# Optimization experiments

Measured on AMD Instinct MI355X. Metric: run time of the kernel, lower is better.

Reference implementation:

```python
import jax, jax.numpy as jnp
import numpy as np

N, E, C_IN, W = 7936, 63488, 5, 64
K, H1, H2 = 8, 64, 16  # kernel size, tgc hidden, gcn out

def _conv1d(x, w, b):
    # x: [N, Cin, L], w: [Cout, Cin, K] -> [N, Cout, L-K+1]
    y = jax.lax.conv_general_dilated(x, w, (1,), 'VALID',
                                     dimension_numbers=('NCH', 'OIH', 'NCH'))
    return y + b[None, :, None]

def _gated_conv(x, w, b, out_ch):
    # Conv1d to 2*out_ch channels, then GLU: P * sigmoid(Q)
    y = _conv1d(x, w, b)
    return y[:, :out_ch] * jax.nn.sigmoid(y[:, out_ch:])

def _gcn(x, edge_index, edge_weight, Wg, bg, num_nodes):
    # x: [T, N, F] (node_dim=-2), GCNConv with self-loops and symmetric norm
    row, col = edge_index[0], edge_index[1]
    loop = jnp.arange(num_nodes, dtype=edge_index.dtype)
    row = jnp.concatenate([row, loop])
    col = jnp.concatenate([col, loop])
    ew = jnp.concatenate([edge_weight, jnp.ones((num_nodes,), x.dtype)])
    deg = jax.ops.segment_sum(ew, col, num_segments=num_nodes)
    dinv = jnp.where(deg > 0, jax.lax.rsqrt(deg), 0.0)
    norm = dinv[row] * ew * dinv[col]              # [E+N]
    xt = jnp.einsum('tnf,fo->tno', x, Wg)          # transform first (F->O)
    msgs = jnp.take(xt, row, axis=1) * norm[None, :, None]  # [T, E+N, O]
    T = x.shape[0]
    out = jnp.zeros((T, num_nodes, Wg.shape[1]), x.dtype).at[:, col, :].add(msgs)
    return out + bg

def setup_inputs() -> dict:
    key = jax.random.key(0)
    ks = jax.random.split(key, 10)
    x = jax.random.normal(ks[0], (N, C_IN, W), jnp.float32)
    edge_index = jax.random.randint(ks[1], (2, E), 0, N, jnp.int64)
    edge_attr = jax.random.uniform(ks[2], (E,), jnp.float32)
    batch = jax.random.randint(ks[3], (N,), 0, 128, jnp.int64)
    s1 = 1.0 / np.sqrt(C_IN * K)
    Wc1 = jax.random.uniform(ks[4], (2 * H1, C_IN, K), jnp.float32, -s1, s1)
    b1 = jax.random.uniform(ks[5], (2 * H1,), jnp.float32, -s1, s1)
    sg = 1.0 / np.sqrt(H1)
    Wg = jax.random.uniform(ks[6], (H1, H2), jnp.float32, -sg, sg)
    bg = jnp.zeros((H2,), jnp.float32)
    s2 = 1.0 / np.sqrt(H2 * K)
    Wc2 = jax.random.uniform(ks[7], (2 * H1, H2, K), jnp.float32, -s2, s2)
    b2 = jax.random.uniform(ks[8], (2 * H1,), jnp.float32, -s2, s2)
    return {'x': x, 'edge_index': edge_index, 'edge_attr': edge_attr,
            'batch': batch, 'Wc1': Wc1, 'b1': b1, 'Wg': Wg, 'bg': bg,
            'Wc2': Wc2, 'b2': b2}

def reference(x, edge_index, edge_attr, batch, Wc1, b1, Wg, bg, Wc2, b2):
    h = _gated_conv(x, Wc1, b1, H1)                # [N, 64, T1]
    h = jnp.transpose(h, (2, 0, 1))                # 'ec cs wc -> wc ec cs'
    h = jax.nn.relu(_gcn(h, edge_index, edge_attr, Wg, bg, x.shape[0]))
    h = jnp.transpose(h, (1, 2, 0))                # 'wc ec cs -> ec cs wc'
    return _gated_conv(h, Wc2, b2, H1)             # [N, 64, T2]
```

## Files before the change

### kernel.cpp

```cpp
#include <hip/hip_runtime.h>
#include <hip/hip_bf16.h>

#define NN 7936
#define EE 63488
#define CIN 5
#define WW 64
#define KK 8
#define H1C 64
#define H2C 16
#define T1 57
#define T2 50
#define FT (T1*H2C)
#define CAP 64
#define GSTR 24

typedef _Float16 half8 __attribute__((ext_vector_type(8)));
typedef _Float16 half4v __attribute__((ext_vector_type(4)));
typedef float f32x4 __attribute__((ext_vector_type(4)));

__device__ __forceinline__ int block_flag(const int* __restrict__ ei,
                                          int* sflag) {
    if (threadIdx.x < 64) {
        int bad = (threadIdx.x < 32) ? (ei[2 * threadIdx.x + 1] != 0) : 0;
        unsigned long long b = __ballot(bad);
        if (threadIdx.x == 0) *sflag = (b == 0ULL) ? 1 : 0;
    }
    __syncthreads();
    return *sflag;
}

__device__ __forceinline__ int load_row(const int* ei, int f, int e) {
    return f ? ei[2 * e] : ei[e];
}
__device__ __forceinline__ int load_col(const int* ei, int f, int e) {
    return f ? ei[2 * (EE + e)] : ei[EE + e];
}

__global__ void k_init(float* __restrict__ deg,
                       const float* __restrict__ Wc2, _Float16* __restrict__ w2p,
                       const float* __restrict__ Wc1, _Float16* __restrict__ w1p,
                       const float* __restrict__ Wg, _Float16* __restrict__ wgp) {
    int b = blockIdx.x;
    if (b < 62) {
        ((int*)deg)[b * 256 + threadIdx.x] = 0;
        return;
    }
    int i = (b - 62) * 256 + threadIdx.x;
    if (i < 16384) {
        int e = i & 7;
        int slot = i >> 3;
        int c  = slot & 15;
        int nt = (slot >> 4) & 7;
        int g  = (slot >> 7) & 3;
        int s  = (slot >> 9) & 3;
        int ci = g * 4 + (e & 3);
        w2p[i] = (_Float16)Wc2[(nt * 16 + c) * 128 + ci * 8 + 2 * s + (e >> 2)];
    } else if (i < 16384 + 8192) {
        int j = i - 16384;
        int e = j & 7;
        int m = (j >> 3) & 127;
        int slg = j >> 10;
        int ci = (slg >> 2) * 4 + (slg & 3);
        int hi = m >> 6;
        int mb = m & 63;
        int mt = mb >> 4, r = mb & 15;
        int sig = hi * 64 + 32 * (mt >> 1) + 8 * (r >> 2) + 4 * (mt & 1) + (r & 3);
        w1p[j] = (ci < CIN) ? (_Float16)Wc1[sig * (CIN * KK) + ci * KK + e]
                            : (_Float16)0.0f;
    } else if (i < 16384 + 8192 + 1024) {
        int j = i - 16384 - 8192;
        int e = j & 7;
        int f = (j >> 3) & 15;
        int slg = j >> 7;
        int c = (slg >> 2) * 32 + (slg & 3) * 8 + e;
        wgp[j] = (_Float16)Wg[c * H2C + f];
    }
}

__global__ __launch_bounds__(256, 3) void k_conv1_fill(
        const float* __restrict__ x, const _Float16* __restrict__ w1p,
        const float* __restrict__ b1, const _Float16* __restrict__ wgp,
        _Float16* __restrict__ xt,
        const int* __restrict__ ei,
        const float* __restrict__ ew, float* __restrict__ deg,
        int* __restrict__ cnt, int2* __restrict__ em) {
    if (blockIdx.x >= NN / 4) {
        __shared__ int sflag;
        int f = block_flag(ei, &sflag);
        int e = (blockIdx.x - NN / 4) * 256 + threadIdx.x;
        if (e < EE) {
            int c = load_col(ei, f, e);
            int r = load_row(ei, f, e);
            float wv = ew[e];
            int pos = atomicAdd(&cnt[c], 1);
            atomicAdd(&deg[c], wv);
            if (pos < CAP)
                em[(c << 6) + pos] = make_int2(r, __float_as_int(wv));
        }
        return;
    }
    int tid = threadIdx.x;
    int w = tid >> 6, lane = tid & 63;
    int lc = lane & 15, lg = lane >> 4;
    int n = blockIdx.x * 4 + w;
    const float* xg = x + (size_t)n * (CIN * WW);

    const half8* w1v = (const half8*)w1p;
    const half8* wgv = (const half8*)wgp;

    half8 av[2][8];
#pragma unroll
    for (int s = 0; s < 2; ++s)
#pragma unroll
        for (int mt = 0; mt < 8; ++mt)
            av[s][mt] = w1v[(s * 4 + lg) * 128 + mt * 16 + lc];
    half8 bw[2];
#pragma unroll
    for (int s2 = 0; s2 < 2; ++s2) bw[s2] = wgv[(s2 * 4 + lg) * 16 + lc];

    const float* xr0 = xg + (size_t)lg * WW;
    const float* xr1 = xg + (size_t)(4 + lg) * WW;
    bool cok1 = (4 + lg) < CIN;

    f32x4 acc2[4];
#pragma unroll
    for (int mt2 = 0; mt2 < 4; ++mt2) acc2[mt2] = (f32x4)0.0f;

#pragma unroll
    for (int nt = 0; nt < 4; ++nt) {
        int t = nt * 16 + lc;
        half8 bf0, bf1;
#pragma unroll
        for (int e = 0; e < 8; ++e) {
            int tp = t + e;
            bf0[e] = (_Float16)((tp < WW) ? xr0[tp] : 0.0f);
            bf1[e] = (_Float16)((cok1 && tp < WW) ? xr1[tp] : 0.0f);
        }
        f32x4 acc[8];
#pragma unroll
        for (int mt = 0; mt < 8; ++mt) acc[mt] = (f32x4)0.0f;
#pragma unroll
        for (int mt = 0; mt < 8; ++mt)
            acc[mt] = __builtin_amdgcn_mfma_f32_16x16x32_f16(av[0][mt], bf0,
                                                             acc[mt], 0, 0, 0);
#pragma unroll
        for (int mt = 0; mt < 8; ++mt)
            acc[mt] = __builtin_amdgcn_mfma_f32_16x16x32_f16(av[1][mt], bf1,
                                                             acc[mt], 0, 0, 0);
        half4v h4[4];
#pragma unroll
        for (int mtp = 0; mtp < 4; ++mtp) {
            int cb = 32 * (mtp >> 1) + 8 * lg + 4 * (mtp & 1);
            float4 bP = *(const float4*)(b1 + cb);
            float4 bQ = *(const float4*)(b1 + 64 + cb);
            f32x4 P = acc[mtp];
            f32x4 Q = acc[mtp + 4];
            half4v hh;
            hh[0] = (_Float16)((P[0] + bP.x) * (1.0f / (1.0f + __expf(-(Q[0] + bQ.x)))));
            hh[1] = (_Float16)((P[1] + bP.y) * (1.0f / (1.0f + __expf(-(Q[1] + bQ.y)))));
            hh[2] = (_Float16)((P[2] + bP.z) * (1.0f / (1.0f + __expf(-(Q[2] + bQ.z)))));
            hh[3] = (_Float16)((P[3] + bP.w) * (1.0f / (1.0f + __expf(-(Q[3] + bQ.w)))));
            h4[mtp] = hh;
        }
#pragma unroll
        for (int s2 = 0; s2 < 2; ++s2) {
            half8 af = __builtin_shufflevector(h4[2 * s2], h4[2 * s2 + 1],
                                               0, 1, 2, 3, 4, 5, 6, 7);
            acc2[nt] = __builtin_amdgcn_mfma_f32_16x16x32_f16(af, bw[s2],
                                                              acc2[nt], 0, 0, 0);
        }
    }

    _Float16* xtn = xt + (size_t)n * FT;
#pragma unroll
    for (int mt2 = 0; mt2 < 4; ++mt2) {
#pragma unroll
        for (int j = 0; j < 4; ++j) {
            int t = mt2 * 16 + 4 * lg + j;
            if (t < T1) xtn[t * 16 + lc] = (_Float16)acc2[mt2][j];
        }
    }
}

__global__ __launch_bounds__(256, 4) void k_gc2(
        const _Float16* __restrict__ xt, const float* __restrict__ deg,
        const int* __restrict__ cnt, const int2* __restrict__ em,
        const float* __restrict__ bg, const _Float16* __restrict__ w2p,
        const float* __restrict__ b2, float* __restrict__ out) {
    __shared__ __align__(16) _Float16 gs2[2][58 * GSTR];
    __shared__ __align__(16) float gout[4][16 * T2];
    int tid = threadIdx.x;
    int w = tid >> 6, lane = tid & 63;
    int lc = lane & 15, lg = lane >> 4;
    int nb = w >> 1, h = w & 1;
    int n = blockIdx.x * 2 + nb;
    bool act = (h == 0) || (lane < 50);
    int idx = (h << 6) + lane;

    float dc = rsqrtf(deg[n] + 1.0f);
    float a[8];
    {
        const half8* xs = (const half8*)(xt + (size_t)n * FT);
        half8 u = (half8)(_Float16)0.0f;
        if (act) u = xs[idx];
#pragma unroll
        for (int j = 0; j < 8; ++j) a[j] = (float)u[j] * dc;
    }
    int beg = n << 6;
    int m = min(cnt[n], CAP);
    int2 rw0 = make_int2(0, 0), rw1 = make_int2(0, 0);
    float dg0 = 0.0f, dg1 = 0.0f;
    half8 c0 = (half8)(_Float16)0.0f;
    if (m > 0) {
        rw0 = em[beg];
        dg0 = deg[rw0.x];
        const half8* xr = (const half8*)(xt + (size_t)rw0.x * FT);
        if (act) c0 = xr[idx];
    }
    if (m > 1) { rw1 = em[beg + 1]; dg1 = deg[rw1.x]; }
    for (int i = 0; i < m; ++i) {
        float wv = __int_as_float(rw0.y) * rsqrtf(dg0 + 1.0f);
        half8 d0 = c0;
        int2 rwn = rw1;
        float dgn = dg1;
        if (i + 2 < m) { rwn = em[beg + i + 2]; dgn = deg[rwn.x]; }
        if (i + 1 < m) {
            const half8* xr = (const half8*)(xt + (size_t)rw1.x * FT);
            c0 = (half8)(_Float16)0.0f;
            if (act) c0 = xr[idx];
        }
        rw0 = rw1; dg0 = dg1; rw1 = rwn; dg1 = dgn;
#pragma unroll
        for (int j = 0; j < 8; ++j) a[j] += (float)d0[j] * wv;
    }

    {
        _Float16* g = gs2[nb];
        int f0 = (lane & 1) * 8;
        int t0 = idx >> 1;
        float4 bgA = *(const float4*)(bg + f0);
        float4 bgB = *(const float4*)(bg + f0 + 4);
        float bv[8] = {bgA.x, bgA.y, bgA.z, bgA.w, bgB.x, bgB.y, bgB.z, bgB.w};
        half8 h0;
#pragma unroll
        for (int j = 0; j < 8; ++j)
            h0[j] = (_Float16)fmaxf(a[j] * dc + bv[j], 0.0f);
        if (act) *(half8*)(g + t0 * GSTR + f0) = h0;
    }
    __syncthreads();

    const _Float16* g = gs2[nb];
    half8 af[4][4];
#pragma unroll
    for (int s = 0; s < 4; ++s)
#pragma unroll
        for (int mt = 0; mt < 4; ++mt) {
            int tb = mt * 16 + lc + 2 * s;
            half4v lo = *(const half4v*)(g + tb * GSTR + lg * 4);
            half4v hh = *(const half4v*)(g + (tb + 1) * GSTR + lg * 4);
            af[s][mt] = __builtin_shufflevector(lo, hh, 0, 1, 2, 3, 4, 5, 6, 7);
        }

    const half8* wsv = (const half8*)w2p;
    float* outn = out + (size_t)n * (H1C * T2);
    float* go = gout[w];
#pragma unroll
    for (int np2 = 0; np2 < 2; ++np2) {
        int ntp = (h << 1) + np2;
        f32x4 aP[4], aQ[4];
#pragma unroll
        for (int mt = 0; mt < 4; ++mt) { aP[mt] = (f32x4)0.0f; aQ[mt] = (f32x4)0.0f; }
#pragma unroll
        for (int s = 0; s < 4; ++s) {
            half8 bP = wsv[(s * 4 + lg) * 128 + ntp * 16 + lc];
            half8 bQ = wsv[(s * 4 + lg) * 128 + (ntp + 4) * 16 + lc];
#pragma unroll
            for (int mt = 0; mt < 4; ++mt) {
                aP[mt] = __builtin_amdgcn_mfma_f32_16x16x32_f16(af[s][mt], bP,
                                                                aP[mt], 0, 0, 0);
                aQ[mt] = __builtin_amdgcn_mfma_f32_16x16x32_f16(af[s][mt], bQ,
                                                                aQ[mt], 0, 0, 0);
            }
        }
        int c = ntp * 16 + lc;
        float bp = b2[c], bq = b2[64 + c];
#pragma unroll
        for (int mt = 0; mt < 4; ++mt) {
#pragma unroll
            for (int e2 = 0; e2 < 4; ++e2) {
                int t = mt * 16 + lg * 4 + e2;
                if (t < T2) {
                    float vv = (aP[mt][e2] + bp) *
                               (1.0f / (1.0f + __expf(-(aQ[mt][e2] + bq))));
                    go[lc * T2 + t] = vv;
                }
            }
        }
        float* dst = outn + ntp * (16 * T2);
#pragma unroll
        for (int i = 0; i < 3; ++i) {
            f32x4 v = *(const f32x4*)(go + i * 256 + lane * 4);
            __builtin_nontemporal_store(v, (f32x4*)(dst + i * 256 + lane * 4));
        }
        if (lane < 8) {
            f32x4 v = *(const f32x4*)(go + 768 + lane * 4);
            __builtin_nontemporal_store(v, (f32x4*)(dst + 768 + lane * 4));
        }
    }
}

extern "C" void kernel_launch(void* const* d_in, const int* in_sizes, int n_in,
                              void* d_out, int out_size, void* d_ws, size_t ws_size,
                              hipStream_t stream) {
    const float* x   = (const float*)d_in[0];
    const int*   ei  = (const int*)d_in[1];
    const float* ea  = (const float*)d_in[2];
    const float* Wc1 = (const float*)d_in[4];
    const float* b1  = (const float*)d_in[5];
    const float* Wg  = (const float*)d_in[6];
    const float* bg  = (const float*)d_in[7];
    const float* Wc2 = (const float*)d_in[8];
    const float* b2  = (const float*)d_in[9];
    float* out = (float*)d_out;

    char* ws = (char*)d_ws;
    size_t off = 0;
    auto alloc = [&](size_t bytes) -> void* {
        void* p = ws + off;
        off += (bytes + 255) & ~(size_t)255;
        return p;
    };
    float*    deg = (float*)alloc((size_t)NN * 4);
    int*      cnt = (int*)alloc((size_t)NN * 4);
    int2*     em  = (int2*)alloc((size_t)NN * CAP * 8);
    _Float16* xt  = (_Float16*)alloc((size_t)NN * FT * 2);
    _Float16* w2p = (_Float16*)alloc((size_t)16384 * 2);
    _Float16* w1p = (_Float16*)alloc((size_t)8192 * 2);
    _Float16* wgp = (_Float16*)alloc((size_t)1024 * 2);
    (void)ws_size; (void)in_sizes; (void)n_in; (void)out_size;

    k_init<<<162, 256, 0, stream>>>(deg, Wc2, w2p, Wc1, w1p, Wg, wgp);
    k_conv1_fill<<<NN / 4 + EE / 256, 256, 0, stream>>>(x, w1p, b1, wgp, xt,
                                                        ei, ea, deg, cnt, em);
    k_gc2<<<NN / 2, 256, 0, stream>>>(xt, deg, cnt, em, bg, w2p, b2, out);
}
```

Before: 104.1 us.

## Read conv1/GCN weights directly in fill kernel, shrink gc2 blocks to one node

The fp16 repacking of Wc1 and Wg moves out of the init kernel. The conv1 kernel now loads and converts those weights straight from the fp32 inputs, which makes the init kernel smaller and drops two workspace buffers. The gather/conv2 kernel now runs one node per 128-thread block instead of two nodes per 256-thread block, with fewer LDS bytes per block and a higher occupancy hint. It also raises wave priority around the MFMA loop. The trade-off is redundant per-wave weight conversion in conv1 and twice as many small blocks for gc2.

```diff
diff --git a/kernel.cpp b/kernel.cpp
--- a/kernel.cpp
+++ b/kernel.cpp
@@ -37,49 +37,26 @@
 }
 
 __global__ void k_init(float* __restrict__ deg,
-                       const float* __restrict__ Wc2, _Float16* __restrict__ w2p,
-                       const float* __restrict__ Wc1, _Float16* __restrict__ w1p,
-                       const float* __restrict__ Wg, _Float16* __restrict__ wgp) {
+                       const float* __restrict__ Wc2, _Float16* __restrict__ w2p) {
     int b = blockIdx.x;
     if (b < 62) {
         ((int*)deg)[b * 256 + threadIdx.x] = 0;
         return;
     }
     int i = (b - 62) * 256 + threadIdx.x;
-    if (i < 16384) {
-        int e = i & 7;
-        int slot = i >> 3;
-        int c  = slot & 15;
-        int nt = (slot >> 4) & 7;
-        int g  = (slot >> 7) & 3;
-        int s  = (slot >> 9) & 3;
-        int ci = g * 4 + (e & 3);
-        w2p[i] = (_Float16)Wc2[(nt * 16 + c) * 128 + ci * 8 + 2 * s + (e >> 2)];
-    } else if (i < 16384 + 8192) {
-        int j = i - 16384;
-        int e = j & 7;
-        int m = (j >> 3) & 127;
-        int slg = j >> 10;
-        int ci = (slg >> 2) * 4 + (slg & 3);
-        int hi = m >> 6;
-        int mb = m & 63;
-        int mt = mb >> 4, r = mb & 15;
-        int sig = hi * 64 + 32 * (mt >> 1) + 8 * (r >> 2) + 4 * (mt & 1) + (r & 3);
-        w1p[j] = (ci < CIN) ? (_Float16)Wc1[sig * (CIN * KK) + ci * KK + e]
-                            : (_Float16)0.0f;
-    } else if (i < 16384 + 8192 + 1024) {
-        int j = i - 16384 - 8192;
-        int e = j & 7;
-        int f = (j >> 3) & 15;
-        int slg = j >> 7;
-        int c = (slg >> 2) * 32 + (slg & 3) * 8 + e;
-        wgp[j] = (_Float16)Wg[c * H2C + f];
-    }
+    int e = i & 7;
+    int slot = i >> 3;
+    int c  = slot & 15;
+    int nt = (slot >> 4) & 7;
+    int g  = (slot >> 7) & 3;
+    int s  = (slot >> 9) & 3;
+    int ci = g * 4 + (e & 3);
+    w2p[i] = (_Float16)Wc2[(nt * 16 + c) * 128 + ci * 8 + 2 * s + (e >> 2)];
 }
 
 __global__ __launch_bounds__(256, 3) void k_conv1_fill(
-        const float* __restrict__ x, const _Float16* __restrict__ w1p,
-        const float* __restrict__ b1, const _Float16* __restrict__ wgp,
+        const float* __restrict__ x, const float* __restrict__ Wc1,
+        const float* __restrict__ b1, const float* __restrict__ Wg,
         _Float16* __restrict__ xt,
         const int* __restrict__ ei,
         const float* __restrict__ ew, float* __restrict__ deg,
@@ -105,18 +82,37 @@
     int n = blockIdx.x * 4 + w;
     const float* xg = x + (size_t)n * (CIN * WW);
 
-    const half8* w1v = (const half8*)w1p;
-    const half8* wgv = (const half8*)wgp;
-
     half8 av[2][8];
 #pragma unroll
-    for (int s = 0; s < 2; ++s)
-#pragma unroll
-        for (int mt = 0; mt < 8; ++mt)
-            av[s][mt] = w1v[(s * 4 + lg) * 128 + mt * 16 + lc];
+    for (int s = 0; s < 2; ++s) {
+        int ci = s * 4 + lg;
+#pragma unroll
+        for (int mt = 0; mt < 8; ++mt) {
+            half8 v = (half8)(_Float16)0.0f;
+            if (ci < CIN) {
+                int mb = mt & 3;
+                int sig = (mt >> 2) * 64 + 32 * (mb >> 1) + 8 * (lc >> 2) +
+                          4 * (mb & 1) + (lc & 3);
+                const float* wr = Wc1 + sig * (CIN * KK) + ci * KK;
+                float4 fA = *(const float4*)(wr);
+                float4 fB = *(const float4*)(wr + 4);
+                v[0] = (_Float16)fA.x; v[1] = (_Float16)fA.y;
+                v[2] = (_Float16)fA.z; v[3] = (_Float16)fA.w;
+                v[4] = (_Float16)fB.x; v[5] = (_Float16)fB.y;
+                v[6] = (_Float16)fB.z; v[7] = (_Float16)fB.w;
+            }
+            av[s][mt] = v;
+        }
+    }
     half8 bw[2];
 #pragma unroll
-    for (int s2 = 0; s2 < 2; ++s2) bw[s2] = wgv[(s2 * 4 + lg) * 16 + lc];
+    for (int s2 = 0; s2 < 2; ++s2) {
+        half8 v;
+#pragma unroll
+        for (int e = 0; e < 8; ++e)
+            v[e] = (_Float16)Wg[(s2 * 32 + lg * 8 + e) * H2C + lc];
+        bw[s2] = v;
+    }
 
     const float* xr0 = xg + (size_t)lg * WW;
     const float* xr1 = xg + (size_t)(4 + lg) * WW;
@@ -182,18 +178,17 @@
     }
 }
 
-__global__ __launch_bounds__(256, 4) void k_gc2(
+__global__ __launch_bounds__(128, 8) void k_gc2(
         const _Float16* __restrict__ xt, const float* __restrict__ deg,
         const int* __restrict__ cnt, const int2* __restrict__ em,
         const float* __restrict__ bg, const _Float16* __restrict__ w2p,
         const float* __restrict__ b2, float* __restrict__ out) {
-    __shared__ __align__(16) _Float16 gs2[2][58 * GSTR];
-    __shared__ __align__(16) float gout[4][16 * T2];
+    __shared__ __align__(16) _Float16 gs2[58 * GSTR];
+    __shared__ __align__(16) float gout[2][16 * T2];
     int tid = threadIdx.x;
-    int w = tid >> 6, lane = tid & 63;
+    int h = tid >> 6, lane = tid & 63;
     int lc = lane & 15, lg = lane >> 4;
-    int nb = w >> 1, h = w & 1;
-    int n = blockIdx.x * 2 + nb;
+    int n = blockIdx.x;
     bool act = (h == 0) || (lane < 50);
     int idx = (h << 6) + lane;
 
@@ -235,7 +230,7 @@
     }
 
     {
-        _Float16* g = gs2[nb];
+        _Float16* g = gs2;
         int f0 = (lane & 1) * 8;
         int t0 = idx >> 1;
         float4 bgA = *(const float4*)(bg + f0);
@@ -249,7 +244,7 @@
     }
     __syncthreads();
 
-    const _Float16* g = gs2[nb];
+    const _Float16* g = gs2;
     half8 af[4][4];
 #pragma unroll
     for (int s = 0; s < 4; ++s)
@@ -263,13 +258,14 @@
 
     const half8* wsv = (const half8*)w2p;
     float* outn = out + (size_t)n * (H1C * T2);
-    float* go = gout[w];
+    float* go = gout[h];
 #pragma unroll
     for (int np2 = 0; np2 < 2; ++np2) {
         int ntp = (h << 1) + np2;
         f32x4 aP[4], aQ[4];
 #pragma unroll
         for (int mt = 0; mt < 4; ++mt) { aP[mt] = (f32x4)0.0f; aQ[mt] = (f32x4)0.0f; }
+        __builtin_amdgcn_s_setprio(1);
 #pragma unroll
         for (int s = 0; s < 4; ++s) {
             half8 bP = wsv[(s * 4 + lg) * 128 + ntp * 16 + lc];
@@ -282,6 +278,7 @@
                                                                 aQ[mt], 0, 0, 0);
             }
         }
+        __builtin_amdgcn_s_setprio(0);
         int c = ntp * 16 + lc;
         float bp = b2[c], bq = b2[64 + c];
 #pragma unroll
@@ -335,12 +332,11 @@
     int2*     em  = (int2*)alloc((size_t)NN * CAP * 8);
     _Float16* xt  = (_Float16*)alloc((size_t)NN * FT * 2);
     _Float16* w2p = (_Float16*)alloc((size_t)16384 * 2);
-    _Float16* w1p = (_Float16*)alloc((size_t)8192 * 2);
-    _Float16* wgp = (_Float16*)alloc((size_t)1024 * 2);
+    (void)alloc(4096);
     (void)ws_size; (void)in_sizes; (void)n_in; (void)out_size;
 
-    k_init<<<162, 256, 0, stream>>>(deg, Wc2, w2p, Wc1, w1p, Wg, wgp);
-    k_conv1_fill<<<NN / 4 + EE / 256, 256, 0, stream>>>(x, w1p, b1, wgp, xt,
+    k_init<<<126, 256, 0, stream>>>(deg, Wc2, w2p);
+    k_conv1_fill<<<NN / 4 + EE / 256, 256, 0, stream>>>(x, Wc1, b1, Wg, xt,
                                                         ei, ea, deg, cnt, em);
-    k_gc2<<<NN / 2, 256, 0, stream>>>(xt, deg, cnt, em, bg, w2p, b2, out);
-}
+    k_gc2<<<NN, 128, 0, stream>>>(xt, deg, cnt, em, bg, w2p, b2, out);
+}
```

After: 207.3 us. +99.1%, slower.
